# Kernel optimization log

Hardware: AMD Instinct MI355X
Metric: run time of the kernel (lower is better)

Reference implementation:

```python
import jax, jax.numpy as jnp
import numpy as np

B, T, V, F = 64, 2, 512, 512  # V == F required by the original loop indexing

def setup_inputs() -> dict:
    key = jax.random.key(0)
    x = jax.random.normal(key, (B, T, V, F), dtype=jnp.float32)
    return {"x": x}

def reference(x):
    # split along time axis into two halves; only the first slice of the first half is used
    xh, _ = jnp.split(x, 2, axis=1)
    x0 = xh[:, 0]  # (B, V, F)
    # Faithful to tf.norm(x[:, 0, i, :], ord=2) with NO axis: Frobenius norm over
    # the whole (batch, feature) slice -> one scalar per vertex.
    n = jnp.sqrt(jnp.sum(x0 * x0, axis=(0, 2)))  # (V,)
    # S[b,i,j] = sum_f x0[b,i,f] * x0[b,j,f]  (inner loop over j covers all V since V==F)
    gram = jnp.einsum('bif,bjf->bij', x0, x0)  # (B, V, V)
    return gram / (n[:, None] * n[None, :])
```

## Files before the change

### kernel.cpp

```cpp
#include <hip/hip_runtime.h>
#include <hip/hip_bf16.h>
#include <math.h>


#define BATCH 64
#define VDIM 512
#define FDIM 512
#define XBS (2 * VDIM * FDIM)
#define OBS (VDIM * VDIM)

typedef __bf16 bf16x8 __attribute__((ext_vector_type(8)));
typedef __bf16 bf16x4 __attribute__((ext_vector_type(4)));
typedef float f32x4 __attribute__((ext_vector_type(4)));

#define BM 128
#define BK 64

#define INVN_OFF 33554432

#define GLL16(g, l)                                                          \
    __builtin_amdgcn_global_load_lds(                                        \
        (const __attribute__((address_space(1))) void*)(g),                  \
        (__attribute__((address_space(3))) void*)(l), 16, 0, 0)

__global__ __launch_bounds__(256) void cvt_norm_kernel(const float* __restrict__ x,
                                                       __bf16* __restrict__ xb,
                                                       float* __restrict__ inv_n) {
    const int v = blockIdx.x;
    const int tid = threadIdx.x;
    float s = 0.f;
    const float4* xf4 = (const float4*)x;
    for (int c = tid; c < 8192; c += 256) {
        int b = c >> 7;
        int f4 = c & 127;
        float4 d = xf4[(size_t)b * (XBS / 4) + (size_t)v * (FDIM / 4) + f4];
        s += d.x * d.x + d.y * d.y + d.z * d.z + d.w * d.w;
        bf16x4 p;
        p[0] = (__bf16)d.x; p[1] = (__bf16)d.y; p[2] = (__bf16)d.z; p[3] = (__bf16)d.w;
        *(bf16x4*)&xb[(size_t)b * (VDIM * FDIM) + (size_t)v * FDIM + f4 * 4] = p;
    }
    #pragma unroll
    for (int off = 32; off > 0; off >>= 1) s += __shfl_down(s, off, 64);
    __shared__ float partial[4];
    if ((tid & 63) == 0) partial[tid >> 6] = s;
    __syncthreads();
    if (tid == 0) {
        float t = partial[0] + partial[1] + partial[2] + partial[3];
        inv_n[v] = 1.0f / sqrtf(t);
    }
}

__global__ __launch_bounds__(256) void gram_kernel(const __bf16* __restrict__ xb,
                                                   const float* __restrict__ inv_n,
                                                   float* __restrict__ out) {
    __shared__ __bf16 As[BM * BK];
    __shared__ __bf16 Bs[BM * BK];

    const int bid = blockIdx.x;
    const int wg = (bid & 7) * 128 + (bid >> 3);
    const int batch = wg >> 4;
    const int tile = wg & 15;
    const int ti = tile >> 2;
    const int tj = tile & 3;

    const __bf16* xbb = xb + (size_t)batch * (VDIM * FDIM);
    const int tid = threadIdx.x;
    const int lane = tid & 63;
    const int wave = tid >> 6;
    const int wr = wave >> 1;
    const int wc = wave & 1;

    const __bf16* gA[4];
    const __bf16* gB[4];
    __bf16* la[4];
    __bf16* lb[4];
    #pragma unroll
    for (int it = 0; it < 4; ++it) {
        int c = it * 256 + tid;
        int row = c >> 3;
        int cs = (c & 7) ^ (row & 7);
        gA[it] = xbb + (size_t)(ti * BM + row) * FDIM + cs * 8;
        gB[it] = xbb + (size_t)(tj * BM + row) * FDIM + cs * 8;
        la[it] = &As[c * 8];
        lb[it] = &Bs[c * 8];
    }

    int offA[2][4], offB[2][4];
    #pragma unroll
    for (int ks = 0; ks < 2; ++ks) {
        #pragma unroll
        for (int m = 0; m < 4; ++m) {
            int rA = wr * 64 + m * 16 + (lane & 15);
            int rB = wc * 64 + m * 16 + (lane & 15);
            int gch = ks * 4 + (lane >> 4);
            offA[ks][m] = rA * (BK * 2) + ((gch ^ (rA & 7)) * 16);
            offB[ks][m] = rB * (BK * 2) + ((gch ^ (rB & 7)) * 16);
        }
    }

    f32x4 acc[4][4];
    #pragma unroll
    for (int m = 0; m < 4; ++m)
        #pragma unroll
        for (int n = 0; n < 4; ++n)
            acc[m][n] = (f32x4){0.f, 0.f, 0.f, 0.f};

    for (int kk = 0; kk < FDIM; kk += BK) {
        #pragma unroll
        for (int it = 0; it < 4; ++it) {
            GLL16(gA[it] + kk, la[it]);
            GLL16(gB[it] + kk, lb[it]);
        }
        __syncthreads();

        #pragma unroll
        for (int ks = 0; ks < 2; ++ks) {
            bf16x8 af[4], bfr[4];
            #pragma unroll
            for (int m = 0; m < 4; ++m) {
                af[m]  = *(const bf16x8*)((const char*)As + offA[ks][m]);
                bfr[m] = *(const bf16x8*)((const char*)Bs + offB[ks][m]);
            }
            #pragma unroll
            for (int m = 0; m < 4; ++m)
                #pragma unroll
                for (int n = 0; n < 4; ++n)
                    acc[m][n] = __builtin_amdgcn_mfma_f32_16x16x32_bf16(af[m], bfr[n], acc[m][n], 0, 0, 0);
        }
        __syncthreads();
    }

    const int rowbase = ti * BM + wr * 64;
    const int colbase = tj * BM + wc * 64;
    float* ob = out + (size_t)batch * OBS;

    float si[16];
    #pragma unroll
    for (int m = 0; m < 4; ++m)
        #pragma unroll
        for (int q = 0; q < 4; ++q)
            si[m * 4 + q] = inv_n[rowbase + m * 16 + (lane >> 4) * 4 + q];

    #pragma unroll
    for (int n = 0; n < 4; ++n) {
        int j = colbase + n * 16 + (lane & 15);
        float sj = inv_n[j];
        #pragma unroll
        for (int m = 0; m < 4; ++m) {
            #pragma unroll
            for (int q = 0; q < 4; ++q) {
                int i = rowbase + m * 16 + (lane >> 4) * 4 + q;
                ob[(size_t)i * VDIM + j] = acc[m][n][q] * si[m * 4 + q] * sj;
            }
        }
    }
}

extern "C" void kernel_launch(void* const* d_in, const int* in_sizes, int n_in,
                              void* d_out, int out_size, void* d_ws, size_t ws_size,
                              hipStream_t stream) {
    const float* x = (const float*)d_in[0];
    float* out = (float*)d_out;
    __bf16* xbf = (__bf16*)d_ws;
    float* inv_n = (float*)((char*)d_ws + INVN_OFF);

    cvt_norm_kernel<<<VDIM, 256, 0, stream>>>(x, xbf, inv_n);
    gram_kernel<<<BATCH * 16, 256, 0, stream>>>(xbf, inv_n, out);
}
```

Measured before the change: 50.06 us.

## Tile conversion kernel per batch block and accumulate norms with atomics

The conversion/norm kernel now runs 1024 blocks, each covering 32 contiguous rows of one batch, instead of 512 blocks that each stride across all batches for a single vertex. Per-row partial squared norms are reduced within groups of 8 lanes and added to a global buffer with atomics. The gram kernel then takes rsqrt of these sums in its epilogue. The aim is more contiguous loads, more parallelism and an XCD-aware block ordering, at the cost of an added memset, float atomics and nondeterministic summation order.

```diff
diff --git a/kernel.cpp b/kernel.cpp
--- a/kernel.cpp
+++ b/kernel.cpp
@@ -16,7 +16,7 @@
 #define BM 128
 #define BK 64
 
-#define INVN_OFF 33554432
+#define NSQ_OFF 33554432
 
 #define GLL16(g, l)                                                          \
     __builtin_amdgcn_global_load_lds(                                        \
@@ -25,33 +25,39 @@
 
 __global__ __launch_bounds__(256) void cvt_norm_kernel(const float* __restrict__ x,
                                                        __bf16* __restrict__ xb,
-                                                       float* __restrict__ inv_n) {
-    const int v = blockIdx.x;
+                                                       float* __restrict__ nsq) {
+    const int bid = blockIdx.x;
+    const int L = (bid & 7) * 128 + (bid >> 3);
+    const int b = L >> 4;
+    const int g = L & 15;
     const int tid = threadIdx.x;
+    const int r = tid >> 3;
+    const int seg = tid & 7;
+
+    const f32x4* src = (const f32x4*)(x + (size_t)b * XBS + (size_t)(g * 32) * FDIM);
+    bf16x4* dst = (bf16x4*)(xb + (size_t)b * (VDIM * FDIM) + (size_t)(g * 32) * FDIM);
+
     float s = 0.f;
-    const float4* xf4 = (const float4*)x;
-    for (int c = tid; c < 8192; c += 256) {
-        int b = c >> 7;
-        int f4 = c & 127;
-        float4 d = xf4[(size_t)b * (XBS / 4) + (size_t)v * (FDIM / 4) + f4];
-        s += d.x * d.x + d.y * d.y + d.z * d.z + d.w * d.w;
+    #pragma unroll
+    for (int k = 0; k < 16; ++k) {
+        int c = r * 128 + seg + k * 8;
+        f32x4 d = src[c];
+        s += d[0] * d[0] + d[1] * d[1] + d[2] * d[2] + d[3] * d[3];
         bf16x4 p;
-        p[0] = (__bf16)d.x; p[1] = (__bf16)d.y; p[2] = (__bf16)d.z; p[3] = (__bf16)d.w;
-        *(bf16x4*)&xb[(size_t)b * (VDIM * FDIM) + (size_t)v * FDIM + f4 * 4] = p;
+        p[0] = (__bf16)d[0]; p[1] = (__bf16)d[1]; p[2] = (__bf16)d[2]; p[3] = (__bf16)d[3];
+        dst[c] = p;
     }
-    #pragma unroll
-    for (int off = 32; off > 0; off >>= 1) s += __shfl_down(s, off, 64);
-    __shared__ float partial[4];
-    if ((tid & 63) == 0) partial[tid >> 6] = s;
+    s += __shfl_xor(s, 1, 64);
+    s += __shfl_xor(s, 2, 64);
+    s += __shfl_xor(s, 4, 64);
+    __shared__ float nl[32];
+    if (seg == 0) nl[r] = s;
     __syncthreads();
-    if (tid == 0) {
-        float t = partial[0] + partial[1] + partial[2] + partial[3];
-        inv_n[v] = 1.0f / sqrtf(t);
-    }
+    if (tid < 32) atomicAdd(&nsq[g * 32 + tid], nl[tid]);
 }
 
 __global__ __launch_bounds__(256) void gram_kernel(const __bf16* __restrict__ xb,
-                                                   const float* __restrict__ inv_n,
+                                                   const float* __restrict__ nsq,
                                                    float* __restrict__ out) {
     __shared__ __bf16 As[BM * BK];
     __shared__ __bf16 Bs[BM * BK];
@@ -139,12 +145,12 @@
     for (int m = 0; m < 4; ++m)
         #pragma unroll
         for (int q = 0; q < 4; ++q)
-            si[m * 4 + q] = inv_n[rowbase + m * 16 + (lane >> 4) * 4 + q];
+            si[m * 4 + q] = rsqrtf(nsq[rowbase + m * 16 + (lane >> 4) * 4 + q]);
 
     #pragma unroll
     for (int n = 0; n < 4; ++n) {
         int j = colbase + n * 16 + (lane & 15);
-        float sj = inv_n[j];
+        float sj = rsqrtf(nsq[j]);
         #pragma unroll
         for (int m = 0; m < 4; ++m) {
             #pragma unroll
@@ -162,8 +168,9 @@
     const float* x = (const float*)d_in[0];
     float* out = (float*)d_out;
     __bf16* xbf = (__bf16*)d_ws;
-    float* inv_n = (float*)((char*)d_ws + INVN_OFF);
+    float* nsq = (float*)((char*)d_ws + NSQ_OFF);
 
-    cvt_norm_kernel<<<VDIM, 256, 0, stream>>>(x, xbf, inv_n);
-    gram_kernel<<<BATCH * 16, 256, 0, stream>>>(xbf, inv_n, out);
+    hipMemsetAsync(nsq, 0, VDIM * sizeof(float), stream);
+    cvt_norm_kernel<<<BATCH * 16, 256, 0, stream>>>(x, xbf, nsq);
+    gram_kernel<<<BATCH * 16, 256, 0, stream>>>(xbf, nsq, out);
 }
```

After: 51.23 us. 2.3% more time.
